# Kernel optimization log

Measured on AMD Instinct MI355X. Metric: run time of the kernel, lower is better.

Reference implementation:

```python
import jax, jax.numpy as jnp
import numpy as np

L = 16            # table_num (levels)
LOG2T = 14
T = 1 << LOG2T    # entries per table
Z = 512           # z_dim
S = 256           # style_dim
IMG = 256         # img_size
RES_MIN, RES_MAX = 16, 256
HID, OUT = 64, 3  # mlp hidden / out dims
B = 8
FDIM = 2 * L      # retrieved feature dim (2 per level)
PRIME = jnp.uint32(2654435761)  # instant-ngp hash prime
GAIN = 1.4142135623730951       # stylegan lrelu gain sqrt(2)
# geometric level resolutions res_min -> res_max
RES = np.floor(RES_MIN * np.exp(np.arange(L) * np.log(RES_MAX / RES_MIN) / (L - 1))).astype(np.float32)


def _lrelu(x):
    return GAIN * jnp.where(x >= 0, x, 0.2 * x)


def _coords():
    c = (jnp.arange(IMG, dtype=jnp.float32) + 0.5) / IMG
    x, y = jnp.meshgrid(c, c, indexing='ij')
    return jnp.stack((x, y), -1).reshape(-1, 2)  # (N, 2), N = IMG*IMG


def _mod_linear(x, s, aw, ab, w, b):
    # StyleGAN2-style modulated linear with demodulation. x: (B,N,in), s: (B,S)
    style = s @ aw + ab                                   # (B, in)
    demod = jax.lax.rsqrt((style ** 2) @ (w ** 2) + 1e-8)  # (B, out)
    return ((x * style[:, None, :]) @ w) * demod[:, None, :] + b


def _forward(z, mw0, mb0, mw1, mb1, mw2, mb2, base_tables, w_mod, b_mod,
             a0w, a0b, w0, bb0, a1w, a1b, w1, bb1, a2w, a2b, w2, bb2):
    s = _lrelu(z @ mw0 + mb0)
    s = _lrelu(s @ mw1 + mb1)
    s = _lrelu(s @ mw2 + mb2)                              # (B, S)
    # style-conditioned hash tables: per-level per-channel modulation of base tables
    scale = 1.0 + (s @ w_mod + b_mod).reshape(-1, L, 1, 2)
    tables = base_tables[None] * scale                     # (B, L, T, 2)

    coords = _coords()                                     # (N, 2)
    offs = jnp.array([[0, 0], [1, 0], [0, 1], [1, 1]], dtype=jnp.uint32)
    feats = []
    for l in range(L):
        pos = coords * RES[l]
        p0 = jnp.floor(pos)
        frac = pos - p0                                    # (N, 2)
        p0i = p0.astype(jnp.uint32)
        cx = p0i[None, :, 0] + offs[:, 0:1]                # (4, N)
        cy = p0i[None, :, 1] + offs[:, 1:2]
        idx = ((cx ^ (cy * PRIME)) & jnp.uint32(T - 1)).astype(jnp.int32)  # (4, N)
        wx = jnp.where(offs[:, 0:1] == 1, frac[None, :, 0], 1.0 - frac[None, :, 0])
        wy = jnp.where(offs[:, 1:2] == 1, frac[None, :, 1], 1.0 - frac[None, :, 1])
        wgt = wx * wy                                      # (4, N)
        tl = tables[:, l]                                  # (B, T, 2)
        f = jnp.take(tl, idx.reshape(-1), axis=1).reshape(tl.shape[0], 4, -1, 2)
        feats.append(jnp.einsum('bcnd,cn->bnd', f, wgt))   # bilinear interp
    h = jnp.concatenate(feats, -1)                         # (B, N, 2L)

    # stacked modulated MLP (3 layers), final tanh, then render to image
    h = _lrelu(_mod_linear(h, s, a0w, a0b, w0, bb0))
    h = _lrelu(_mod_linear(h, s, a1w, a1b, w1, bb1))
    h = jnp.tanh(_mod_linear(h, s, a2w, a2b, w2, bb2))     # (B, N, 3)
    return h.reshape(-1, IMG, IMG, OUT).transpose(0, 3, 1, 2)


def setup_inputs() -> dict:
    key = jax.random.key(0)
    ks = jax.random.split(key, 12)
    nrm = lambda k, sh, sc: jax.random.normal(k, sh, jnp.float32) * sc
    inp = {}
    inp['z'] = jax.random.normal(ks[0], (B, Z), jnp.float32)
    inp['mw0'] = nrm(ks[1], (Z, S), 1 / np.sqrt(Z)); inp['mb0'] = jnp.zeros((S,), jnp.float32)
    inp['mw1'] = nrm(ks[2], (S, S), 1 / np.sqrt(S)); inp['mb1'] = jnp.zeros((S,), jnp.float32)
    inp['mw2'] = nrm(ks[3], (S, S), 1 / np.sqrt(S)); inp['mb2'] = jnp.zeros((S,), jnp.float32)
    inp['base_tables'] = nrm(ks[4], (L, T, 2), 0.1)
    inp['w_mod'] = nrm(ks[5], (S, L * 2), 1 / np.sqrt(S)); inp['b_mod'] = jnp.zeros((L * 2,), jnp.float32)
    inp['a0w'] = nrm(ks[6], (S, FDIM), 1 / np.sqrt(S)); inp['a0b'] = jnp.ones((FDIM,), jnp.float32)
    inp['w0'] = nrm(ks[7], (FDIM, HID), 1 / np.sqrt(FDIM)); inp['bb0'] = jnp.zeros((HID,), jnp.float32)
    inp['a1w'] = nrm(ks[8], (S, HID), 1 / np.sqrt(S)); inp['a1b'] = jnp.ones((HID,), jnp.float32)
    inp['w1'] = nrm(ks[9], (HID, HID), 1 / np.sqrt(HID)); inp['bb1'] = jnp.zeros((HID,), jnp.float32)
    inp['a2w'] = nrm(ks[10], (S, HID), 1 / np.sqrt(S)); inp['a2b'] = jnp.ones((HID,), jnp.float32)
    inp['w2'] = nrm(ks[11], (HID, OUT), 1 / np.sqrt(HID)); inp['bb2'] = jnp.zeros((OUT,), jnp.float32)
    return inp


def reference(z, mw0, mb0, mw1, mb1, mw2, mb2, base_tables, w_mod, b_mod,
              a0w, a0b, w0, bb0, a1w, a1b, w1, bb1, a2w, a2b, w2, bb2):
    return _forward(z, mw0, mb0, mw1, mb1, mw2, mb2, base_tables, w_mod, b_mod,
                    a0w, a0b, w0, bb0, a1w, a1b, w1, bb1, a2w, a2b, w2, bb2)
```

## Files before the change

kernel.cpp:

```cpp
#include <hip/hip_runtime.h>
#include <hip/hip_bf16.h>

#define NLVL 16
#define TSZ  16384
#define NB   8

typedef _Float16 h8 __attribute__((ext_vector_type(8)));
typedef float    f4 __attribute__((ext_vector_type(4)));

#define MFMA16(A,B,C) __builtin_amdgcn_mfma_f32_16x16x32_f16(A,B,C,0,0,0)
#define GAINF 1.41421356237309515f

__device__ const float RES_TAB[16] = {
  16.f, 19.f, 23.f, 27.f, 33.f, 40.f, 48.f, 58.f,
  70.f, 84.f, 101.f, 122.f, 147.f, 176.f, 212.f, 255.f
};

__device__ __forceinline__ float lrelu(float x) {
  float v = x < 0.0f ? 0.2f * x : x;
  return GAINF * v;
}
__device__ __forceinline__ float act(float x) { return fmaxf(x, 0.2f * x); }

__device__ __forceinline__ float tanh_fast(float x) {
  float t = __builtin_amdgcn_exp2f(x * 2.8853900817779268f);
  return 1.0f - 2.0f * __builtin_amdgcn_rcpf(t + 1.0f);
}

__device__ __forceinline__ unsigned pk(float a, float b) {
  union { decltype(__builtin_amdgcn_cvt_pkrtz(0.f, 0.f)) h; unsigned u; } U;
  U.h = __builtin_amdgcn_cvt_pkrtz(a, b);
  return U.u;
}

__device__ __forceinline__ void hash4(const float* __restrict__ bt,
                                      int n, int l0, float* g8)
{
  const float inv = 1.0f / 256.0f;
  float cx = ((n >> 8) + 0.5f) * inv;
  float cy = ((n & 255) + 0.5f) * inv;
#pragma unroll
  for (int j = 0; j < 4; ++j) {
    float res = RES_TAB[l0 + j];
    float px = cx * res, py = cy * res;
    float fx0 = floorf(px), fy0 = floorf(py);
    float fx = px - fx0, fy = py - fy0;
    unsigned x0 = (unsigned)fx0, y0 = (unsigned)fy0;
    unsigned hy0 = y0 * 2654435761u;
    unsigned hy1 = (y0 + 1u) * 2654435761u;
    unsigned i00 = (x0 ^ hy0) & 16383u;
    unsigned i10 = ((x0 + 1u) ^ hy0) & 16383u;
    unsigned i01 = (x0 ^ hy1) & 16383u;
    unsigned i11 = ((x0 + 1u) ^ hy1) & 16383u;
    const float2* tb = (const float2*)(bt + (size_t)(l0 + j) * (TSZ * 2));
    float2 f00 = tb[i00], f10 = tb[i10], f01 = tb[i01], f11 = tb[i11];
    float wx0 = 1.0f - fx, wy0 = 1.0f - fy;
    float w00 = wx0 * wy0, w10 = fx * wy0, w01 = wx0 * fy, w11 = fx * fy;
    g8[2 * j]     = w00 * f00.x + w10 * f10.x + w01 * f01.x + w11 * f11.x;
    g8[2 * j + 1] = w00 * f00.y + w10 * f10.y + w01 * f01.y + w11 * f11.y;
  }
}

__device__ __forceinline__ void hash_features(const float* __restrict__ bt,
                                              int n, float* g)
{
#pragma unroll
  for (int q = 0; q < 4; ++q) hash4(bt, n, q * 4, g + 8 * q);
}

__device__ __forceinline__ void map_layer(const float* __restrict__ xs_in,
                                          float* __restrict__ out_lds,
                                          const float* __restrict__ W,
                                          const float* __restrict__ bias,
                                          int K, int t,
                                          float* __restrict__ part)
{
  const int j4 = (t & 63) * 4;
  const int ks = t >> 6;
  const int chunk = K >> 2;
  const int kb = ks * chunk;
  f4 a0 = {0,0,0,0}, a1 = {0,0,0,0}, a2 = {0,0,0,0}, a3 = {0,0,0,0};
#pragma unroll 4
  for (int k = 0; k < chunk; k += 4) {
    f4 w0 = *(const f4*)&W[(kb + k + 0) * 256 + j4];
    f4 w1 = *(const f4*)&W[(kb + k + 1) * 256 + j4];
    f4 w2 = *(const f4*)&W[(kb + k + 2) * 256 + j4];
    f4 w3 = *(const f4*)&W[(kb + k + 3) * 256 + j4];
    float x0 = xs_in[kb + k + 0], x1 = xs_in[kb + k + 1];
    float x2 = xs_in[kb + k + 2], x3 = xs_in[kb + k + 3];
    a0 += x0 * w0; a1 += x1 * w1; a2 += x2 * w2; a3 += x3 * w3;
  }
  *(f4*)&part[ks * 256 + j4] = (a0 + a1) + (a2 + a3);
  __syncthreads();
  {
    float v = part[t] + part[256 + t] + part[512 + t] + part[768 + t];
    out_lds[t] = lrelu(bias[t] + v);
  }
  __syncthreads();
}

__global__ void __launch_bounds__(256) k_pre(
    const float* __restrict__ z,
    const float* __restrict__ mw0, const float* __restrict__ mb0,
    const float* __restrict__ mw1, const float* __restrict__ mb1,
    const float* __restrict__ mw2, const float* __restrict__ mb2,
    const float* __restrict__ bt,
    const float* __restrict__ w_mod, const float* __restrict__ b_mod,
    const float* __restrict__ a0w, const float* __restrict__ a0b,
    const float* __restrict__ w0,
    const float* __restrict__ a1w, const float* __restrict__ a1b,
    const float* __restrict__ w1,
    const float* __restrict__ a2w, const float* __restrict__ a2b,
    const float* __restrict__ w2,
    _Float16* __restrict__ W0h, _Float16* __restrict__ W1h,
    _Float16* __restrict__ W2h, _Float16* __restrict__ ghf)
{
  __shared__ float xs[512];
  __shared__ float sA[256], sB[256];
  __shared__ float part[1024];
  __shared__ float st0[32], scf[32], st1[64], st2[64];
  __shared__ float dm0[64], dm1[64], dm2[3];

  const int t = threadIdx.x;

  if (blockIdx.x >= 8) {
    int hb = blockIdx.x - 8;
    int lg = hb & 3;
    int n  = (hb >> 2) * 256 + t;
    float g8[8];
    hash4(bt, n, lg * 4, g8);
    int tile = n >> 4, c = n & 15;
    union { unsigned u[4]; uint4 v; } U;
    U.u[0] = pk(g8[0], g8[1]);
    U.u[1] = pk(g8[2], g8[3]);
    U.u[2] = pk(g8[4], g8[5]);
    U.u[3] = pk(g8[6], g8[7]);
    *(uint4*)&ghf[(size_t)tile * 512 + (lg * 16 + c) * 8] = U.v;
    return;
  }

  const int b = blockIdx.x;

  for (int k = t; k < 512; k += 256) xs[k] = z[b * 512 + k];
  __syncthreads();

  map_layer(xs, sA, mw0, mb0, 512, t, part);
  map_layer(sA, sB, mw1, mb1, 256, t, part);
  map_layer(sB, xs, mw2, mb2, 256, t, part);
  const float* ss = xs;

  {
    const int j = t & 31, kb = (t >> 5) * 32;
    float am = 0.f, as = 0.f;
#pragma unroll 8
    for (int k = 0; k < 32; ++k) {
      float sv = ss[kb + k];
      am = fmaf(sv, w_mod[(kb + k) * 32 + j], am);
      as = fmaf(sv, a0w[(kb + k) * 32 + j], as);
    }
    part[t] = am; part[256 + t] = as;
  }
  {
    const int j = t & 63, kb = (t >> 6) * 64;
    float v1 = 0.f, v2 = 0.f;
#pragma unroll 8
    for (int k = 0; k < 64; ++k) {
      float sv = ss[kb + k];
      v1 = fmaf(sv, a1w[(kb + k) * 64 + j], v1);
      v2 = fmaf(sv, a2w[(kb + k) * 64 + j], v2);
    }
    part[512 + t] = v1; part[768 + t] = v2;
  }
  __syncthreads();
  if (t < 32) {
    float am = b_mod[t], as = a0b[t];
#pragma unroll
    for (int q = 0; q < 8; ++q) { am += part[q * 32 + t]; as += part[256 + q * 32 + t]; }
    scf[t] = 1.0f + am; st0[t] = as;
  }
  if (t >= 128 && t < 192) {
    int j = t - 128;
    float v1 = a1b[j], v2 = a2b[j];
#pragma unroll
    for (int q = 0; q < 4; ++q) { v1 += part[512 + q * 64 + j]; v2 += part[768 + q * 64 + j]; }
    st1[j] = v1; st2[j] = v2;
  }
  __syncthreads();

  if (t < 64) {
    float acc = 1e-8f;
    for (int i = 0; i < 32; ++i) { float p = st0[i] * w0[i * 64 + t]; acc = fmaf(p, p, acc); }
    dm0[t] = 1.0f / sqrtf(acc);
  }
  if (t >= 64 && t < 128) {
    int j = t - 64; float acc = 1e-8f;
    for (int k = 0; k < 64; ++k) { float p = st1[k] * w1[k * 64 + j]; acc = fmaf(p, p, acc); }
    dm1[j] = 1.0f / sqrtf(acc);
  }
  if (t >= 192 && t < 195) {
    int ch = t - 192; float acc = 1e-8f;
    for (int k = 0; k < 64; ++k) { float p = st2[k] * w2[k * 3 + ch]; acc = fmaf(p, p, acc); }
    dm2[ch] = 1.0f / sqrtf(acc);
  }
  __syncthreads();

  for (int f = t; f < 2048; f += 256) {
    int j = f >> 5, i = f & 31;
    W0h[b * 2048 + f] = (_Float16)(scf[i] * st0[i] * w0[i * 64 + j] * dm0[j]);
  }
  for (int f = t; f < 4096; f += 256) {
    int j2 = f >> 6, k = f & 63;
    W1h[b * 4096 + f] = (_Float16)(GAINF * st1[k] * w1[k * 64 + j2] * dm1[j2]);
  }
  for (int f = t; f < 1024; f += 256) {
    int ch = f >> 6, k = f & 63;
    W2h[b * 1024 + f] = (ch < 3) ? (_Float16)(GAINF * st2[k] * w2[k * 3 + ch] * dm2[ch])
                                 : (_Float16)0.0f;
  }
}

__device__ __forceinline__ void st4(_Float16* L, int pix, int jb, f4 v) {
  int ks = jb ^ ((pix & 7) << 3);
  union { unsigned u[2]; uint2 v2; } U;
  U.u[0] = pk(v[0], v[1]); U.u[1] = pk(v[2], v[3]);
  *(uint2*)(L + pix * 64 + ks) = U.v2;
}
__device__ __forceinline__ h8 ldf(const _Float16* L, int pix, int kb) {
  int ks = kb ^ ((pix & 7) << 3);
  return *(const h8*)(L + pix * 64 + ks);
}

template <int FUSED>
__global__ void __launch_bounds__(256) k_mlp(
    const _Float16* __restrict__ W0h, const _Float16* __restrict__ W1h,
    const _Float16* __restrict__ W2h, const _Float16* __restrict__ ghf,
    const float* __restrict__ bt,
    const float* __restrict__ bb0, const float* __restrict__ bb1,
    const float* __restrict__ bb2, float* __restrict__ out)
{
  __shared__ _Float16 lds[4][4096];
  __shared__ _Float16 hb[FUSED ? 8192 : 8];

  const int t = threadIdx.x;
  const int w = t >> 6, lane = t & 63;
  const int c = lane & 15, g = lane >> 4;
  const int b = blockIdx.y;
  const int pixb = blockIdx.x * 256 + w * 64;
  const int tile0 = pixb >> 4;
  _Float16* L = lds[w];

  if constexpr (FUSED) {
    float gl[32];
    hash_features(bt, blockIdx.x * 256 + t, gl);
    int tl = t >> 4, cl = t & 15;
#pragma unroll
    for (int gg = 0; gg < 4; ++gg) {
      union { unsigned u[4]; uint4 v; } U;
      U.u[0] = pk(gl[8 * gg + 0], gl[8 * gg + 1]);
      U.u[1] = pk(gl[8 * gg + 2], gl[8 * gg + 3]);
      U.u[2] = pk(gl[8 * gg + 4], gl[8 * gg + 5]);
      U.u[3] = pk(gl[8 * gg + 6], gl[8 * gg + 7]);
      *(uint4*)&hb[tl * 512 + (gg * 16 + cl) * 8] = U.v;
    }
    __syncthreads();
  }

  h8 A0[4], A1[4][2], A2[2];
#pragma unroll
  for (int jt = 0; jt < 4; ++jt)
    A0[jt] = *(const h8*)&W0h[b * 2048 + (jt * 16 + c) * 32 + 8 * g];
#pragma unroll
  for (int jt = 0; jt < 4; ++jt)
#pragma unroll
    for (int kf = 0; kf < 2; ++kf)
      A1[jt][kf] = *(const h8*)&W1h[b * 4096 + (jt * 16 + c) * 64 + kf * 32 + 8 * g];
#pragma unroll
  for (int kf = 0; kf < 2; ++kf)
    A2[kf] = *(const h8*)&W2h[b * 1024 + c * 64 + kf * 32 + 8 * g];

  f4 bv0[4], bv1[4], bv2;
#pragma unroll
  for (int jt = 0; jt < 4; ++jt) {
    bv0[jt] = *(const f4*)&bb0[jt * 16 + 4 * g];
    bv1[jt] = *(const f4*)&bb1[jt * 16 + 4 * g];
  }
  if (g == 0) { bv2 = f4{bb2[0], bb2[1], bb2[2], 0.0f}; }
  else        { bv2 = f4{0.0f, 0.0f, 0.0f, 0.0f}; }

  f4 acc[4][4];
#pragma unroll
  for (int pt = 0; pt < 4; ++pt) {
    h8 Bh;
    if constexpr (FUSED) {
      Bh = *(const h8*)&hb[(w * 4 + pt) * 512 + lane * 8];
    } else {
      Bh = *(const h8*)&ghf[(size_t)(tile0 + pt) * 512 + lane * 8];
    }
#pragma unroll
    for (int jt = 0; jt < 4; ++jt)
      acc[jt][pt] = MFMA16(A0[jt], Bh, bv0[jt]);
  }

#pragma unroll
  for (int jt = 0; jt < 4; ++jt)
#pragma unroll
    for (int pt = 0; pt < 4; ++pt) {
      f4 v = acc[jt][pt];
#pragma unroll
      for (int r = 0; r < 4; ++r) v[r] = act(v[r]);
      st4(L, pt * 16 + c, jt * 16 + 4 * g, v);
    }

  f4 acc1[4][4];
#pragma unroll
  for (int pt = 0; pt < 4; ++pt) {
    h8 Bf0 = ldf(L, pt * 16 + c, 0 * 32 + 8 * g);
    h8 Bf1 = ldf(L, pt * 16 + c, 1 * 32 + 8 * g);
#pragma unroll
    for (int jt = 0; jt < 4; ++jt) {
      f4 a = MFMA16(A1[jt][0], Bf0, bv1[jt]);
      acc1[jt][pt] = MFMA16(A1[jt][1], Bf1, a);
    }
  }

#pragma unroll
  for (int jt = 0; jt < 4; ++jt)
#pragma unroll
    for (int pt = 0; pt < 4; ++pt) {
      f4 v = acc1[jt][pt];
#pragma unroll
      for (int r = 0; r < 4; ++r) v[r] = act(v[r]);
      st4(L, pt * 16 + c, jt * 16 + 4 * g, v);
    }

#pragma unroll
  for (int pt = 0; pt < 4; ++pt) {
    h8 Bf0 = ldf(L, pt * 16 + c, 0 * 32 + 8 * g);
    h8 Bf1 = ldf(L, pt * 16 + c, 1 * 32 + 8 * g);
    f4 a = MFMA16(A2[0], Bf0, bv2);
    a = MFMA16(A2[1], Bf1, a);
    if (g == 0) {
      int pix = pixb + pt * 16 + c;
#pragma unroll
      for (int r = 0; r < 3; ++r)
        out[((b * 3 + r) << 16) + pix] = tanh_fast(a[r]);
    }
  }
}

extern "C" void kernel_launch(void* const* d_in, const int* in_sizes, int n_in,
                              void* d_out, int out_size, void* d_ws, size_t ws_size,
                              hipStream_t stream)
{
  const float* z    = (const float*)d_in[0];
  const float* mw0  = (const float*)d_in[1];
  const float* mb0  = (const float*)d_in[2];
  const float* mw1  = (const float*)d_in[3];
  const float* mb1  = (const float*)d_in[4];
  const float* mw2  = (const float*)d_in[5];
  const float* mb2  = (const float*)d_in[6];
  const float* bt   = (const float*)d_in[7];
  const float* wmod = (const float*)d_in[8];
  const float* bmod = (const float*)d_in[9];
  const float* a0w  = (const float*)d_in[10];
  const float* a0b  = (const float*)d_in[11];
  const float* w0   = (const float*)d_in[12];
  const float* bb0  = (const float*)d_in[13];
  const float* a1w  = (const float*)d_in[14];
  const float* a1b  = (const float*)d_in[15];
  const float* w1   = (const float*)d_in[16];
  const float* bb1  = (const float*)d_in[17];
  const float* a2w  = (const float*)d_in[18];
  const float* a2b  = (const float*)d_in[19];
  const float* w2   = (const float*)d_in[20];
  const float* bb2  = (const float*)d_in[21];

  char* ws = (char*)d_ws;
  _Float16* W0h = (_Float16*)(ws);
  _Float16* W1h = (_Float16*)(ws + 32768);
  _Float16* W2h = (_Float16*)(ws + 98304);
  _Float16* ghf = (_Float16*)(ws + 114688);
  float* out = (float*)d_out;

  if (ws_size >= (size_t)4308992) {
    k_pre<<<8 + 1024, 256, 0, stream>>>(z, mw0, mb0, mw1, mb1, mw2, mb2, bt,
                                        wmod, bmod, a0w, a0b, w0,
                                        a1w, a1b, w1, a2w, a2b, w2,
                                        W0h, W1h, W2h, ghf);
    k_mlp<0><<<dim3(256, NB), 256, 0, stream>>>(W0h, W1h, W2h, ghf, bt,
                                                bb0, bb1, bb2, out);
  } else {
    k_pre<<<8, 256, 0, stream>>>(z, mw0, mb0, mw1, mb1, mw2, mb2, bt,
                                 wmod, bmod, a0w, a0b, w0,
                                 a1w, a1b, w1, a2w, a2b, w2,
                                 W0h, W1h, W2h, ghf);
    k_mlp<1><<<dim3(256, NB), 256, 0, stream>>>(W0h, W1h, W2h, ghf, bt,
                                                bb0, bb1, bb2, out);
  }
}
```

Baseline: 49.61 us.

## Stage per-level hash table in LDS and restructure hash-grid precompute blocks

The hash-feature precompute blocks now handle one level each: they load that level's whole table into shared memory as fp16 pairs, then every thread does its bilinear lookups from LDS instead of scattered global gathers. The grid drops from 1024 to 128 hash blocks, and each thread covers 32 pixels along x for a fixed y. The modulation reductions in the style blocks are also vectorised with float4 loads and a wider partial-sum split. In exchange, 64KB of LDS per block limits occupancy, table values are rounded to fp16 before interpolation, and the fp16 packing switches from round-toward-zero to round-to-nearest-even.

```diff
diff --git a/kernel.cpp b/kernel.cpp
--- a/kernel.cpp
+++ b/kernel.cpp
@@ -30,6 +30,11 @@
 __device__ __forceinline__ unsigned pk(float a, float b) {
   union { decltype(__builtin_amdgcn_cvt_pkrtz(0.f, 0.f)) h; unsigned u; } U;
   U.h = __builtin_amdgcn_cvt_pkrtz(a, b);
+  return U.u;
+}
+__device__ __forceinline__ unsigned pk_rne(float a, float b) {
+  union { _Float16 h[2]; unsigned u; } U;
+  U.h[0] = (_Float16)a; U.h[1] = (_Float16)b;
   return U.u;
 }
 
@@ -115,29 +120,78 @@
     _Float16* __restrict__ W0h, _Float16* __restrict__ W1h,
     _Float16* __restrict__ W2h, _Float16* __restrict__ ghf)
 {
-  __shared__ float xs[512];
-  __shared__ float sA[256], sB[256];
-  __shared__ float part[1024];
-  __shared__ float st0[32], scf[32], st1[64], st2[64];
-  __shared__ float dm0[64], dm1[64], dm2[3];
+  __shared__ __align__(16) unsigned smem[16384];
 
   const int t = threadIdx.x;
 
   if (blockIdx.x >= 8) {
-    int hb = blockIdx.x - 8;
-    int lg = hb & 3;
-    int n  = (hb >> 2) * 256 + t;
-    float g8[8];
-    hash4(bt, n, lg * 4, g8);
-    int tile = n >> 4, c = n & 15;
-    union { unsigned u[4]; uint4 v; } U;
-    U.u[0] = pk(g8[0], g8[1]);
-    U.u[1] = pk(g8[2], g8[3]);
-    U.u[2] = pk(g8[4], g8[5]);
-    U.u[3] = pk(g8[6], g8[7]);
-    *(uint4*)&ghf[(size_t)tile * 512 + (lg * 16 + c) * 8] = U.v;
+    const int hb  = blockIdx.x - 8;
+    const int lvl = hb & 15;
+    const int pg  = hb >> 4;
+    const int gg  = lvl >> 2;
+    const int sub = 2 * (lvl & 3);
+
+    const float4* tb4 = (const float4*)(bt + (size_t)lvl * (TSZ * 2));
+#pragma unroll 8
+    for (int i = 0; i < 32; ++i) {
+      float4 v = tb4[i * 256 + t];
+      int e = (i * 256 + t) * 2;
+      smem[e]     = pk_rne(v.x, v.y);
+      smem[e + 1] = pk_rne(v.z, v.w);
+    }
+    __syncthreads();
+
+    const float res = RES_TAB[lvl];
+    const float inv = 1.0f / 256.0f;
+    float cy = (t + 0.5f) * inv;
+    float py = cy * res;
+    float fy0 = floorf(py);
+    float fy = py - fy0;
+    unsigned y0 = (unsigned)fy0;
+    unsigned hy0 = y0 * 2654435761u;
+    unsigned hy1 = (y0 + 1u) * 2654435761u;
+    float wy0 = 1.0f - fy;
+
+    const int xbase = pg * 32;
+    const int cc = t & 15, th = t >> 4;
+#pragma unroll 4
+    for (int i = 0; i < 32; ++i) {
+      float cx = (xbase + i + 0.5f) * inv;
+      float px = cx * res;
+      float fx0 = floorf(px);
+      float fx = px - fx0;
+      unsigned x0 = (unsigned)fx0;
+      unsigned i00 = (x0 ^ hy0) & 16383u;
+      unsigned i10 = ((x0 + 1u) ^ hy0) & 16383u;
+      unsigned i01 = (x0 ^ hy1) & 16383u;
+      unsigned i11 = ((x0 + 1u) ^ hy1) & 16383u;
+      union { unsigned u; _Float16 h[2]; } e00, e10, e01, e11;
+      e00.u = smem[i00]; e10.u = smem[i10];
+      e01.u = smem[i01]; e11.u = smem[i11];
+      float wx0 = 1.0f - fx;
+      float w00 = wx0 * wy0, w10 = fx * wy0, w01 = wx0 * fy, w11 = fx * fy;
+      float gx = w00 * (float)e00.h[0] + w10 * (float)e10.h[0]
+               + w01 * (float)e01.h[0] + w11 * (float)e11.h[0];
+      float gy = w00 * (float)e00.h[1] + w10 * (float)e10.h[1]
+               + w01 * (float)e01.h[1] + w11 * (float)e11.h[1];
+      int tile = pg * 512 + i * 16 + th;
+      *(unsigned*)&ghf[(size_t)tile * 512 + (gg * 16 + cc) * 8 + sub] =
+          pk_rne(gx, gy);
+    }
     return;
   }
+
+  float* xs   = (float*)smem;
+  float* sA   = (float*)smem + 512;
+  float* sB   = (float*)smem + 768;
+  float* part = (float*)smem + 1024;
+  float* st0  = (float*)smem + 3072;
+  float* scf  = (float*)smem + 3104;
+  float* st1  = (float*)smem + 3136;
+  float* st2  = (float*)smem + 3200;
+  float* dm0  = (float*)smem + 3264;
+  float* dm1  = (float*)smem + 3328;
+  float* dm2  = (float*)smem + 3392;
 
   const int b = blockIdx.x;
 
@@ -150,39 +204,43 @@
   const float* ss = xs;
 
   {
-    const int j = t & 31, kb = (t >> 5) * 32;
-    float am = 0.f, as = 0.f;
-#pragma unroll 8
-    for (int k = 0; k < 32; ++k) {
+    const int jg = (t & 7) * 4, kc = t >> 3, kb = kc * 8;
+    f4 am = {0,0,0,0}, as = {0,0,0,0};
+#pragma unroll
+    for (int k = 0; k < 8; ++k) {
       float sv = ss[kb + k];
-      am = fmaf(sv, w_mod[(kb + k) * 32 + j], am);
-      as = fmaf(sv, a0w[(kb + k) * 32 + j], as);
-    }
-    part[t] = am; part[256 + t] = as;
-  }
-  {
-    const int j = t & 63, kb = (t >> 6) * 64;
-    float v1 = 0.f, v2 = 0.f;
-#pragma unroll 8
-    for (int k = 0; k < 64; ++k) {
-      float sv = ss[kb + k];
-      v1 = fmaf(sv, a1w[(kb + k) * 64 + j], v1);
-      v2 = fmaf(sv, a2w[(kb + k) * 64 + j], v2);
-    }
-    part[512 + t] = v1; part[768 + t] = v2;
+      am += sv * *(const f4*)&w_mod[(kb + k) * 32 + jg];
+      as += sv * *(const f4*)&a0w[(kb + k) * 32 + jg];
+    }
+    *(f4*)&part[kc * 32 + jg] = am;
+    *(f4*)&part[1024 + kc * 32 + jg] = as;
   }
   __syncthreads();
   if (t < 32) {
     float am = b_mod[t], as = a0b[t];
 #pragma unroll
-    for (int q = 0; q < 8; ++q) { am += part[q * 32 + t]; as += part[256 + q * 32 + t]; }
+    for (int q = 0; q < 32; ++q) { am += part[q * 32 + t]; as += part[1024 + q * 32 + t]; }
     scf[t] = 1.0f + am; st0[t] = as;
   }
+  __syncthreads();
+  {
+    const int jg = (t & 15) * 4, kc = t >> 4, kb = kc * 16;
+    f4 v1 = {0,0,0,0}, v2 = {0,0,0,0};
+#pragma unroll
+    for (int k = 0; k < 16; ++k) {
+      float sv = ss[kb + k];
+      v1 += sv * *(const f4*)&a1w[(kb + k) * 64 + jg];
+      v2 += sv * *(const f4*)&a2w[(kb + k) * 64 + jg];
+    }
+    *(f4*)&part[kc * 64 + jg] = v1;
+    *(f4*)&part[1024 + kc * 64 + jg] = v2;
+  }
+  __syncthreads();
   if (t >= 128 && t < 192) {
     int j = t - 128;
     float v1 = a1b[j], v2 = a2b[j];
 #pragma unroll
-    for (int q = 0; q < 4; ++q) { v1 += part[512 + q * 64 + j]; v2 += part[768 + q * 64 + j]; }
+    for (int q = 0; q < 16; ++q) { v1 += part[q * 64 + j]; v2 += part[1024 + q * 64 + j]; }
     st1[j] = v1; st2[j] = v2;
   }
   __syncthreads();
@@ -383,10 +441,10 @@
   float* out = (float*)d_out;
 
   if (ws_size >= (size_t)4308992) {
-    k_pre<<<8 + 1024, 256, 0, stream>>>(z, mw0, mb0, mw1, mb1, mw2, mb2, bt,
-                                        wmod, bmod, a0w, a0b, w0,
-                                        a1w, a1b, w1, a2w, a2b, w2,
-                                        W0h, W1h, W2h, ghf);
+    k_pre<<<8 + 128, 256, 0, stream>>>(z, mw0, mb0, mw1, mb1, mw2, mb2, bt,
+                                       wmod, bmod, a0w, a0b, w0,
+                                       a1w, a1b, w1, a2w, a2b, w2,
+                                       W0h, W1h, W2h, ghf);
     k_mlp<0><<<dim3(256, NB), 256, 0, stream>>>(W0h, W1h, W2h, ghf, bt,
                                                 bb0, bb1, bb2, out);
   } else {
```

Result: faster. 45.22 us (-8.9%).
